# Performance work log

Hardware: AMD Instinct MI355X
Metric: run time of the kernel (lower is better)

The kernel has to match this reference:

```python
import jax, jax.numpy as jnp
import numpy as np

B, T, D_IN, D_OUT, N_FILT, MAX_T = 4, 2048, 512, 512, 24, 2048


def _hankel_filters(max_t: int, k: int) -> np.ndarray:
    # Z_{ij} = 2 / ((i+j)^3 - (i+j)), 1-indexed; top-|eig| eigenvectors
    idx = np.arange(1, max_t + 1, dtype=np.float64)
    ij = idx[None, :] + idx[:, None]
    Z = 2.0 / (ij ** 3 - ij)
    w, v = np.linalg.eigh(Z)
    top = np.argsort(-np.abs(w))[:k]
    return v[:, top].astype(np.float32)  # (max_t, k)


def setup_inputs() -> dict:
    key = jax.random.key(0)
    kx, km = jax.random.split(key)
    x = jax.random.normal(kx, (B, T, D_IN), dtype=jnp.float32)
    filters = jnp.asarray(_hankel_filters(MAX_T, N_FILT))  # (MAX_T, N)
    # nn.Linear weight is (d_out, d_in); stacked -> (N, d_out, d_in)
    scale = 1.0 / np.sqrt(D_IN)
    M_weights = jax.random.uniform(km, (N_FILT, D_OUT, D_IN), dtype=jnp.float32,
                                   minval=-scale, maxval=scale)
    return {"x": x, "filters": filters, "M_weights": M_weights}


def reference(x, filters, M_weights):
    Tlen = x.shape[1]
    phi = filters[:Tlen]                       # (T, N)
    phi_e = phi[None, :, :, None]              # (1, T, N, 1)
    weighted = phi_e * x[:, :, None, :]        # (B, T, N, D_in)
    csum = jnp.cumsum(weighted, axis=1)        # causal cumulative projection
    # per-filter rectangular projection: (B,T,N,f) x (N,o,f) -> (B,T,N,o)
    modulated = jnp.einsum('btnf,nof->btno', csum, M_weights)
    return (phi_e * modulated).sum(axis=2)     # (B, T, D_out)
```

## Files before the change

### kernel.cpp

```cpp
#include <hip/hip_runtime.h>
#include <stdint.h>

#define BQ 4
#define TT 2048
#define DF 512
#define DOUT 512
#define NF 24
#define CHF 8

typedef __attribute__((ext_vector_type(8))) short short8;
typedef __attribute__((ext_vector_type(4))) float f32x4;

typedef __attribute__((address_space(3))) uint8_t       lds_u8;
typedef __attribute__((address_space(1))) const uint8_t glb_u8;

__device__ __forceinline__ float bf2f(unsigned short u) {
    union { unsigned int i; float f; } v; v.i = ((unsigned int)u) << 16; return v.f;
}
__device__ __forceinline__ unsigned short f2bf(float f) {
    union { float f; unsigned int i; } v; v.f = f;
    unsigned int r = v.i + 0x7FFFu + ((v.i >> 16) & 1u);
    return (unsigned short)(r >> 16);
}
__device__ __forceinline__ float lo16f(unsigned int u) { return __uint_as_float(u << 16); }
__device__ __forceinline__ float hi16f(unsigned int u) { return __uint_as_float(u & 0xffff0000u); }

__device__ __forceinline__ int plaus16(unsigned int h) {
    unsigned int e = (h >> 7) & 0xffu;
    return (e >= 97u && e <= 141u) || ((h & 0x7fffu) == 0u);
}

__global__ void k_detect(const unsigned int* __restrict__ X, int* __restrict__ flag)
{
    const int lane = threadIdx.x;
    int cnt = 0;
#pragma unroll
    for (int i = 0; i < 4; ++i) {
        unsigned int w = X[lane * 4 + i];
        cnt += (plaus16(w >> 16) && plaus16(w & 0xffffu)) ? 1 : 0;
    }
    for (int off = 32; off > 0; off >>= 1) cnt += __shfl_down(cnt, off);
    if (lane == 0) *flag = (cnt < 180) ? 1 : 0;
}

__global__ __launch_bounds__(256) void k_convf(
    const void* __restrict__ src, float* __restrict__ dst,
    const int* __restrict__ flag, int n)
{
    const int isf32 = *flag;
    int i = blockIdx.x * 256 + threadIdx.x;
    const int stride = gridDim.x * 256;
    for (; i < n; i += stride)
        dst[i] = isf32 ? ((const float*)src)[i]
                       : bf2f(((const unsigned short*)src)[i]);
}

__global__ __launch_bounds__(256) void k_prep(
    const void* __restrict__ X, const void* __restrict__ Mw,
    const void* __restrict__ Fil,
    unsigned short* __restrict__ Xbf, unsigned short* __restrict__ Mbf,
    float* __restrict__ Fw, int n4x, int n4m, int n4f)
{
    __shared__ int sflag;
    const int tid = threadIdx.x;
    if (tid < 64) {
        int cnt = 0;
        const unsigned int* Xu = (const unsigned int*)X;
#pragma unroll
        for (int i = 0; i < 4; ++i) {
            unsigned int wd = Xu[tid * 4 + i];
            cnt += (plaus16(wd >> 16) && plaus16(wd & 0xffffu)) ? 1 : 0;
        }
        for (int off = 32; off > 0; off >>= 1) cnt += __shfl_down(cnt, off);
        if (tid == 0) sflag = (cnt < 180) ? 1 : 0;
    }
    __syncthreads();
    const int isf32 = sflag;

    const int total = n4x + n4m + n4f;
    for (int i = blockIdx.x * 256 + tid; i < total; i += gridDim.x * 256) {
        if (i < n4x) {
            ushort4 o;
            if (isf32) {
                float4 v = ((const float4*)X)[i];
                o.x = f2bf(v.x); o.y = f2bf(v.y); o.z = f2bf(v.z); o.w = f2bf(v.w);
            } else {
                o = ((const ushort4*)X)[i];
            }
            ((ushort4*)Xbf)[i] = o;
        } else if (i < n4x + n4m) {
            const int j = i - n4x;
            ushort4 o;
            if (isf32) {
                float4 v = ((const float4*)Mw)[j];
                o.x = f2bf(v.x); o.y = f2bf(v.y); o.z = f2bf(v.z); o.w = f2bf(v.w);
            } else {
                o = ((const ushort4*)Mw)[j];
            }
            ((ushort4*)Mbf)[j] = o;
        } else {
            const int j = i - n4x - n4m;
            if (isf32) {
                ((float4*)Fw)[j] = ((const float4*)Fil)[j];
            } else {
                ushort4 u = ((const ushort4*)Fil)[j];
                ((float4*)Fw)[j] = make_float4(bf2f(u.x), bf2f(u.y),
                                               bf2f(u.z), bf2f(u.w));
            }
        }
    }
}

__global__ __launch_bounds__(256, 3) void k_gemm_fast(
    const unsigned short* __restrict__ X,
    const unsigned short* __restrict__ Mw,
    const float* __restrict__ Fw,
    unsigned short* __restrict__ Z,
    float* __restrict__ Cs,
    int r0)
{
    __shared__ unsigned short sAB[128 * 136];
    __shared__ float sPhi[128];
    unsigned short* const sC = sAB;

    const int tid  = threadIdx.x;
    const int lane = tid & 63;
    const int w    = tid >> 6;
    const int wm   = w & 1, wn = w >> 1;
    const int tm   = blockIdx.x;
    const int on0  = blockIdx.y * 128;
    const int n    = blockIdx.z;

    const int rowg0 = r0 + tm * 128;
    if (tid < 128)
        sPhi[tid] = Fw[((rowg0 + tid) & (TT - 1)) * NF + n];

    const unsigned short* Ag = X + (size_t)rowg0 * DF;
    const unsigned short* Bg = Mw + (size_t)n * DOUT * DF + (size_t)on0 * DF;

    auto stage = [&](int kt, int buf) {
        const unsigned short* Ak = Ag + kt * 32;
        const unsigned short* Bk = Bg + kt * 32;
        lds_u8* base = (lds_u8*)sAB + buf * 16384;
#pragma unroll
        for (int i = 0; i < 2; ++i) {
            const int cbase = i * 256 + w * 64;
            const int c = cbase + lane;
            const int r = c >> 2, qs = c & 3;
            const int qg = qs ^ ((r >> 1) & 3);
            __builtin_amdgcn_global_load_lds(
                (const glb_u8*)(Ak + (size_t)r * DF + qg * 8),
                base + cbase * 16, 16, 0, 0);
            __builtin_amdgcn_global_load_lds(
                (const glb_u8*)(Bk + (size_t)r * DF + qg * 8),
                base + 8192 + cbase * 16, 16, 0, 0);
        }
    };

    f32x4 acc[4][4];
#pragma unroll
    for (int i = 0; i < 4; i++)
#pragma unroll
        for (int j = 0; j < 4; j++) acc[i][j] = (f32x4){0.f, 0.f, 0.f, 0.f};

    stage(0, 0);
    __syncthreads();

    const int lr = lane & 15;
    const int q  = lane >> 4;
    const int qsw = (q ^ ((lr >> 1) & 3)) * 8;

    for (int kt = 0; kt < DF / 32; ++kt) {
        const int cur = kt & 1;
        if (kt < DF / 32 - 1) stage(kt + 1, cur ^ 1);

        const unsigned short* sAc = sAB + cur * 8192;
        const unsigned short* sBc = sAc + 4096;
        short8 a[4], b[4];
#pragma unroll
        for (int i = 0; i < 4; i++)
            a[i] = *(const short8*)&sAc[(wm * 64 + i * 16 + lr) * 32 + qsw];
#pragma unroll
        for (int j = 0; j < 4; j++)
            b[j] = *(const short8*)&sBc[(wn * 64 + j * 16 + lr) * 32 + qsw];
#pragma unroll
        for (int i = 0; i < 4; i++)
#pragma unroll
            for (int j = 0; j < 4; j++)
                acc[i][j] = __builtin_amdgcn_mfma_f32_16x16x32_bf16(
                    a[i], b[j], acc[i][j], 0, 0, 0);

        __syncthreads();
    }

    const int rb = (lane >> 4) * 4;
#pragma unroll
    for (int i = 0; i < 4; i++)
#pragma unroll
        for (int j = 0; j < 4; j++)
#pragma unroll
            for (int r = 0; r < 4; r++) {
                int row = wm * 64 + i * 16 + rb + r;
                sC[row * 136 + wn * 64 + j * 16 + (lane & 15)] =
                    f2bf(acc[i][j][r] * sPhi[row]);
            }
    __syncthreads();

#pragma unroll
    for (int it = 0; it < 8; ++it) {
        int row = it * 16 + (tid >> 4);
        int col = (tid & 15) * 8;
        uint4 v = *(const uint4*)&sC[row * 136 + col];
        *(uint4*)&Z[((size_t)(tm * 128 + row) * NF + n) * 512 + on0 + col] = v;
    }

    {
        const int ci  = tid >> 4;
        const int col = (tid & 15) * 8;
        float s0=0.f,s1=0.f,s2=0.f,s3=0.f,s4=0.f,s5=0.f,s6=0.f,s7=0.f;
#pragma unroll
        for (int r = 0; r < CHF; ++r) {
            uint4 v = *(const uint4*)&sC[(ci * CHF + r) * 136 + col];
            s0 += lo16f(v.x); s1 += hi16f(v.x);
            s2 += lo16f(v.y); s3 += hi16f(v.y);
            s4 += lo16f(v.z); s5 += hi16f(v.z);
            s6 += lo16f(v.w); s7 += hi16f(v.w);
        }
        float* cp = &Cs[((size_t)(tm * 16 + ci) * NF + n) * 512 + on0 + col];
        *(float4*)cp       = make_float4(s0, s1, s2, s3);
        *(float4*)(cp + 4) = make_float4(s4, s5, s6, s7);
    }
}

__global__ __launch_bounds__(256, 2) void k_gemm(
    const void* __restrict__ Xv, const void* __restrict__ Mv,
    const void* __restrict__ Fv, const int* __restrict__ flag,
    unsigned short* __restrict__ Z, int r0, int o0, int W)
{
    __shared__ unsigned short sA[128 * 32];
    __shared__ unsigned short sB[128 * 32];
    __shared__ unsigned short sC[128 * 136];
    __shared__ float sPhi[128];

    const int isf32 = *flag;
    const int tid  = threadIdx.x;
    const int lane = tid & 63;
    const int w    = tid >> 6;
    const int wm   = w & 1, wn = w >> 1;
    const int tm   = blockIdx.x;
    const int on0  = o0 + blockIdx.y * 128;
    const int n    = blockIdx.z;

    const int rowg0 = r0 + tm * 128;
    if (tid < 128) {
        int t = (rowg0 + tid) & (TT - 1);
        sPhi[tid] = isf32 ? ((const float*)Fv)[t * NF + n]
                          : bf2f(((const unsigned short*)Fv)[t * NF + n]);
    }

    const unsigned short* Ah = (const unsigned short*)Xv + (size_t)rowg0 * DF;
    const unsigned short* Bh = (const unsigned short*)Mv +
        (size_t)n * DOUT * DF + (size_t)on0 * DF;
    const float* Af = (const float*)Xv + (size_t)rowg0 * DF;
    const float* Bf = (const float*)Mv + (size_t)n * DOUT * DF + (size_t)on0 * DF;

    f32x4 acc[4][4];
#pragma unroll
    for (int i = 0; i < 4; i++)
#pragma unroll
        for (int j = 0; j < 4; j++) acc[i][j] = (f32x4){0.f, 0.f, 0.f, 0.f};

    for (int kt = 0; kt < DF / 32; ++kt) {
        __syncthreads();
        if (!isf32) {
            const unsigned short* Ak = Ah + kt * 32;
            const unsigned short* Bk = Bh + kt * 32;
#pragma unroll
            for (int i = 0; i < 2; ++i) {
                const int c = i * 256 + tid;
                const int r = c >> 2, cc = (c & 3) * 8;
                *(short8*)&sA[r * 32 + cc] = *(const short8*)(Ak + (size_t)r * DF + cc);
                *(short8*)&sB[r * 32 + cc] = *(const short8*)(Bk + (size_t)r * DF + cc);
            }
        } else {
            const float* Ak = Af + kt * 32;
            const float* Bk = Bf + kt * 32;
#pragma unroll
            for (int i = 0; i < 2; ++i) {
                const int c = i * 256 + tid;
                const int r = c >> 2, cc = (c & 3) * 8;
                float4 a0 = *(const float4*)(Ak + (size_t)r * DF + cc);
                float4 a1 = *(const float4*)(Ak + (size_t)r * DF + cc + 4);
                float4 b0 = *(const float4*)(Bk + (size_t)r * DF + cc);
                float4 b1 = *(const float4*)(Bk + (size_t)r * DF + cc + 4);
                short8 sa, sb;
                sa[0]=(short)f2bf(a0.x); sa[1]=(short)f2bf(a0.y);
                sa[2]=(short)f2bf(a0.z); sa[3]=(short)f2bf(a0.w);
                sa[4]=(short)f2bf(a1.x); sa[5]=(short)f2bf(a1.y);
                sa[6]=(short)f2bf(a1.z); sa[7]=(short)f2bf(a1.w);
                sb[0]=(short)f2bf(b0.x); sb[1]=(short)f2bf(b0.y);
                sb[2]=(short)f2bf(b0.z); sb[3]=(short)f2bf(b0.w);
                sb[4]=(short)f2bf(b1.x); sb[5]=(short)f2bf(b1.y);
                sb[6]=(short)f2bf(b1.z); sb[7]=(short)f2bf(b1.w);
                *(short8*)&sA[r * 32 + cc] = sa;
                *(short8*)&sB[r * 32 + cc] = sb;
            }
        }
        __syncthreads();

        const int lr = lane & 15;
        const int lk = (lane >> 4) * 8;
        short8 a[4], b[4];
#pragma unroll
        for (int i = 0; i < 4; i++)
            a[i] = *(const short8*)&sA[(wm * 64 + i * 16 + lr) * 32 + lk];
#pragma unroll
        for (int j = 0; j < 4; j++)
            b[j] = *(const short8*)&sB[(wn * 64 + j * 16 + lr) * 32 + lk];
#pragma unroll
        for (int i = 0; i < 4; i++)
#pragma unroll
            for (int j = 0; j < 4; j++)
                acc[i][j] = __builtin_amdgcn_mfma_f32_16x16x32_bf16(
                    a[i], b[j], acc[i][j], 0, 0, 0);
    }

    const int rb = (lane >> 4) * 4;
#pragma unroll
    for (int i = 0; i < 4; i++)
#pragma unroll
        for (int j = 0; j < 4; j++)
#pragma unroll
            for (int r = 0; r < 4; r++) {
                int row = wm * 64 + i * 16 + rb + r;
                sC[row * 136 + wn * 64 + j * 16 + (lane & 15)] =
                    f2bf(acc[i][j][r] * sPhi[row]);
            }
    __syncthreads();
#pragma unroll
    for (int it = 0; it < 8; ++it) {
        int row = it * 16 + (tid >> 4);
        int col = (tid & 15) * 8;
        uint4 v = *(const uint4*)&sC[row * 136 + col];
        *(uint4*)&Z[((size_t)(tm * 128 + row) * NF + n) * W + (on0 - o0) + col] = v;
    }
}

__global__ __launch_bounds__(256, 2) void k_csum(
    const unsigned short* __restrict__ Z, float* __restrict__ Cs,
    int W, int CHs)
{
    const int c = blockIdx.x, n = blockIdx.y, tid = threadIdx.x;
    const unsigned short* p = Z + ((size_t)(c * CHs) * NF + n) * W + tid * 2;
    float sx = 0.f, sy = 0.f;
#pragma unroll 8
    for (int t = 0; t < CHs; ++t) {
        unsigned int u = *(const unsigned int*)(p + (size_t)t * NF * W);
        sx += lo16f(u);
        sy += hi16f(u);
    }
    float2* q = (float2*)&Cs[((size_t)c * NF + n) * W + tid * 2];
    *q = make_float2(sx, sy);
}

__global__ __launch_bounds__(256, 4) void k_prefix(
    float* __restrict__ Cs, float* __restrict__ Gc,
    int W, int rr, int nch, int nbat)
{
    __shared__ float2 sPart[4][64];
    const int tid  = threadIdx.x;
    const int wv   = tid >> 6, lane = tid & 63;
    const int obw  = W >> 7;
    const int perB = NF * obw;
    const int gw   = blockIdx.x;
    const int b    = gw / perB;
    const int rest = gw % perB;
    const int n    = rest / obw;
    const int ob   = rest % obw;
    const int opair = ob * 64 + lane;

    float* base = Cs + (size_t)b * nch * NF * W + (size_t)n * W + opair * 2;
    const size_t cstride = (size_t)NF * W;
    const int Q  = nch >> 2;
    const int c0 = wv * Q;
    const int end = c0 + Q;

    float sx = 0.f, sy = 0.f;
    for (int c = c0; c < end; ++c) {
        float2 v = *(const float2*)(base + (size_t)c * cstride);
        sx += v.x; sy += v.y;
    }
    sPart[wv][lane] = make_float2(sx, sy);
    __syncthreads();

    float cx = 0.f, cy = 0.f;
    if (nbat == 1 && rr != 0) {
        float2 gv = *(const float2*)&Gc[(size_t)n * DOUT + opair * 2];
        cx = gv.x; cy = gv.y;
    }
    for (int w2 = 0; w2 < wv; ++w2) {
        float2 p = sPart[w2][lane];
        cx += p.x; cy += p.y;
    }

    int c = c0;
    if (Q >= 16) {
        float2 v[8], nx[8];
#pragma unroll
        for (int k = 0; k < 8; ++k)
            v[k] = *(float2*)(base + (size_t)(c + k) * cstride);
        for (; c + 16 <= end; c += 8) {
#pragma unroll
            for (int k = 0; k < 8; ++k)
                nx[k] = *(float2*)(base + (size_t)(c + 8 + k) * cstride);
#pragma unroll
            for (int k = 0; k < 8; ++k) {
                float2* p = (float2*)(base + (size_t)(c + k) * cstride);
                float2 t = v[k];
                *p = make_float2(cx, cy);
                cx += t.x; cy += t.y;
                v[k] = nx[k];
            }
        }
#pragma unroll
        for (int k = 0; k < 8; ++k) {
            float2* p = (float2*)(base + (size_t)(c + k) * cstride);
            float2 t = v[k];
            *p = make_float2(cx, cy);
            cx += t.x; cy += t.y;
        }
        c += 8;
    }
    for (; c < end; ++c) {
        float2* p = (float2*)(base + (size_t)c * cstride);
        float2 t = *p;
        *p = make_float2(cx, cy);
        cx += t.x; cy += t.y;
    }

    if (nbat == 1 && wv == 3)
        *(float2*)&Gc[(size_t)n * DOUT + opair * 2] = make_float2(cx, cy);
}

#define JLIST(F) F(0) F(1) F(2) F(3) F(4) F(5)

__global__ __launch_bounds__(256, 8) void k_scan(
    const unsigned short* __restrict__ Z, const float* __restrict__ Cs,
    const float* __restrict__ Fw, float* __restrict__ Out,
    int r0, int o0, int W, int CHs)
{
    __shared__ float sPhi[32 * NF];
    __shared__ float2 sP[4][8][64];
    const int cg = blockIdx.x, tid = threadIdx.x;
    const int g = tid >> 6, op = tid & 63;
    const int ng0 = g * 6;
    const int c2  = (blockIdx.y * 64 + op) * 2;
    const int act = (c2 + 2 <= W);
    const int c2u = act ? c2 : (W - 2);
    const int t0g = r0 + cg * CHs;
    const int t0 = t0g & (TT - 1);
    for (int i = tid; i < CHs * NF; i += 256)
        sPhi[i] = Fw[(t0 + i / NF) * NF + (i % NF)];
    __syncthreads();

#define DECLG(j) float gx##j, gy##j;
    JLIST(DECLG)
#define INITG(j) { float2 v = *(const float2*)&Cs[((size_t)cg * NF + ng0 + j) * W + c2u]; \
                   gx##j = v.x; gy##j = v.y; }
    JLIST(INITG)

    const unsigned short* zp = Z + ((size_t)cg * CHs * NF + ng0) * W + c2u;
    float* outb = Out + (size_t)t0g * DOUT + o0 + c2;
    for (int tb = 0; tb < CHs; tb += 8) {
#pragma unroll
        for (int tt = 0; tt < 8; ++tt) {
            float ax = 0.f, ay = 0.f;
            const float* php = &sPhi[(tb + tt) * NF + ng0];
#define UPDG(j) { unsigned int u = *(const unsigned int*)(zp + (size_t)j * W); \
                  gx##j += lo16f(u); gy##j += hi16f(u); \
                  float ph = php[j]; ax += ph * gx##j; ay += ph * gy##j; }
            JLIST(UPDG)
            sP[g][tt][op] = make_float2(ax, ay);
            zp += (size_t)NF * W;
        }
        __syncthreads();
#pragma unroll
        for (int k = 0; k < 2; ++k) {
            const int tt = g * 2 + k;
            float2 p0 = sP[0][tt][op], p1 = sP[1][tt][op],
                   p2 = sP[2][tt][op], p3 = sP[3][tt][op];
            if (act)
                *(float2*)(outb + (size_t)(tb + tt) * DOUT) =
                    make_float2(p0.x + p1.x + p2.x + p3.x,
                                p0.y + p1.y + p2.y + p3.y);
        }
        __syncthreads();
    }
}

extern "C" void kernel_launch(void* const* d_in, const int* in_sizes, int n_in,
                              void* d_out, int out_size, void* d_ws, size_t ws_size,
                              hipStream_t stream)
{
    const void* X = d_in[0]; const void* Fil = d_in[1]; const void* Mw = d_in[2];
    for (int i = 0; i < n_in && i < 3; ++i) {
        if (in_sizes[i] == BQ * TT * DF)        X   = d_in[i];
        else if (in_sizes[i] == TT * NF)        Fil = d_in[i];
        else if (in_sizes[i] == NF * DOUT * DF) Mw  = d_in[i];
    }
    float* Out = (float*)d_out;

    const size_t offF = 256;
    const size_t nbF  = (size_t)TT * NF * 4;
    const size_t off0 = offF + nbF;
    const size_t nbX  = (size_t)BQ * TT * DF * 2;
    const size_t nbM  = (size_t)NF * DOUT * DF * 2;
    const size_t nbGc = (size_t)NF * DOUT * 4;

    int* flag = (int*)d_ws;
    float* Fw = (float*)((char*)d_ws + offF);

    const int n4x = BQ * TT * DF / 4;
    const int n4m = NF * DOUT * DF / 4;
    const int n4f = TT * NF / 4;

    for (int G = BQ; G >= 2; G >>= 1) {
        const size_t zB  = (size_t)G * TT * NF * 512 * 2;
        const size_t csB = (size_t)(G * TT / CHF) * NF * 512 * 4;
        if (off0 + nbX + nbM + zB + csB > ws_size) continue;

        unsigned short* Xbf = (unsigned short*)((char*)d_ws + off0);
        unsigned short* Mbf = (unsigned short*)((char*)Xbf + nbX);
        unsigned short* Z   = (unsigned short*)((char*)Mbf + nbM);
        float* Cs = (float*)((char*)Z + zB);

        hipLaunchKernelGGL(k_prep, dim3(2048), dim3(256), 0, stream,
                           X, Mw, Fil, Xbf, Mbf, Fw, n4x, n4m, n4f);

        const int nch = TT / CHF;
        for (int b0 = 0; b0 < BQ; b0 += G) {
            hipLaunchKernelGGL(k_gemm_fast, dim3(G * TT / 128, 4, NF), dim3(256),
                               0, stream, Xbf, Mbf, Fw, Z, Cs, b0 * TT);
            hipLaunchKernelGGL(k_prefix, dim3(G * NF * 4), dim3(256),
                               0, stream, Cs, (float*)nullptr, 512, 0, nch, G);
            hipLaunchKernelGGL(k_scan, dim3(G * nch, 4), dim3(256), 0, stream,
                               Z, Cs, Fw, Out, b0 * TT, 0, 512, CHF);
        }
        return;
    }

    {
        static const int rts[5] = {2048, 1024, 512, 256, 128};
        int RT = 0;
        for (int ri = 0; ri < 5; ++ri) {
            size_t need = off0 + nbX + nbM
                        + (size_t)rts[ri] * NF * 512 * 2
                        + (size_t)(rts[ri] / CHF) * NF * 512 * 4 + nbGc;
            if (need <= ws_size) { RT = rts[ri]; break; }
        }
        if (RT > 0) {
            unsigned short* Xbf = (unsigned short*)((char*)d_ws + off0);
            unsigned short* Mbf = (unsigned short*)((char*)Xbf + nbX);
            unsigned short* Z   = (unsigned short*)((char*)Mbf + nbM);
            float* Cs = (float*)((char*)Z + (size_t)RT * NF * 512 * 2);
            float* Gc = (float*)((char*)Cs + (size_t)(RT / CHF) * NF * 512 * 4);

            hipLaunchKernelGGL(k_prep, dim3(2048), dim3(256), 0, stream,
                               X, Mw, Fil, Xbf, Mbf, Fw, n4x, n4m, n4f);

            const int nrr = TT / RT, nch = RT / CHF;
            for (int b = 0; b < BQ; ++b) {
                for (int rr = 0; rr < nrr; ++rr) {
                    const int r0 = b * TT + rr * RT;
                    hipLaunchKernelGGL(k_gemm_fast, dim3(RT / 128, 4, NF), dim3(256),
                                       0, stream, Xbf, Mbf, Fw, Z, Cs, r0);
                    hipLaunchKernelGGL(k_prefix, dim3(NF * 4), dim3(256),
                                       0, stream, Cs, Gc, 512, rr, nch, 1);
                    hipLaunchKernelGGL(k_scan, dim3(nch, 4), dim3(256), 0, stream,
                                       Z, Cs, Fw, Out, r0, 0, 512, CHF);
                }
            }
            return;
        }
    }

    hipLaunchKernelGGL(k_detect, dim3(1), dim3(64), 0, stream,
                       (const unsigned int*)X, flag);
    hipLaunchKernelGGL(k_convf, dim3(192), dim3(256), 0, stream,
                       Fil, Fw, flag, TT * NF);

    static const int cRT[7] = {2048, 1024, 512, 256, 128, 128, 128};
    static const int cW[7]  = {512, 512, 512, 512, 512, 256, 128};
    int RTs = 128, W = 128;
    for (int ci = 0; ci < 7; ++ci) {
        size_t need = off0 + (size_t)cRT[ci] * NF * cW[ci] * 2
                    + (size_t)(cRT[ci] / 32) * NF * cW[ci] * 4 + nbGc;
        if (need <= ws_size) { RTs = cRT[ci]; W = cW[ci]; break; }
    }
    unsigned short* Z = (unsigned short*)((char*)d_ws + off0);
    float* Cs = (float*)((char*)Z + (size_t)RTs * NF * W * 2);
    float* Gc = (float*)((char*)Cs + (size_t)(RTs / 32) * NF * W * 4);

    const int nrr = TT / RTs, nch = RTs / 32;
    for (int b = 0; b < BQ; ++b) {
        for (int o0 = 0; o0 < DOUT; o0 += W) {
            for (int rr = 0; rr < nrr; ++rr) {
                const int r0 = b * TT + rr * RTs;
                hipLaunchKernelGGL(k_gemm, dim3(RTs / 128, W / 128, NF), dim3(256),
                                   0, stream, X, Mw, Fil, flag, Z, r0, o0, W);
                hipLaunchKernelGGL(k_csum, dim3(nch, NF), dim3(W / 2), 0, stream,
                                   Z, Cs, W, 32);
                hipLaunchKernelGGL(k_prefix, dim3(NF * (W / 128)), dim3(256),
                                   0, stream, Cs, Gc, W, rr, nch, 1);
                hipLaunchKernelGGL(k_scan, dim3(nch, W / 128), dim3(256),
                                   0, stream, Z, Cs, Fw, Out, r0, o0, W, 32);
            }
        }
    }
}
```

Before: 319.4 us.

## Fuse intra-chunk scan into GEMM epilogue, drop Z intermediate, add apply kernel

The GEMM kernel now loops over all 24 filters inside one block of 64 rows, with the per-filter phi scaling and the within-chunk prefix sum (via shuffles) done in registers. The intra-chunk output contribution is accumulated directly into Out, and only the chunk sums are written to Cs. This removes the large bf16 Z intermediate and the scan kernel's reread of it. A new k_apply kernel adds the cross-chunk carry contributions after the prefix pass. The trade-offs are a smaller 64-row tile, per-filter epilogue overhead inside the main loop, and a read-modify-write of Out.

```diff
diff --git a/kernel.cpp b/kernel.cpp
--- a/kernel.cpp
+++ b/kernel.cpp
@@ -111,17 +111,16 @@
     }
 }
 
-__global__ __launch_bounds__(256, 3) void k_gemm_fast(
+__global__ __launch_bounds__(256, 3) void k_gemm_ns(
     const unsigned short* __restrict__ X,
     const unsigned short* __restrict__ Mw,
     const float* __restrict__ Fw,
-    unsigned short* __restrict__ Z,
     float* __restrict__ Cs,
+    float* __restrict__ Out,
     int r0)
 {
-    __shared__ unsigned short sAB[128 * 136];
-    __shared__ float sPhi[128];
-    unsigned short* const sC = sAB;
+    __shared__ unsigned short sAB[2 * 6144];
+    __shared__ float sPhi2[NF * 64];
 
     const int tid  = threadIdx.x;
     const int lane = tid & 63;
@@ -129,19 +128,28 @@
     const int wm   = w & 1, wn = w >> 1;
     const int tm   = blockIdx.x;
     const int on0  = blockIdx.y * 128;
-    const int n    = blockIdx.z;
-
-    const int rowg0 = r0 + tm * 128;
-    if (tid < 128)
-        sPhi[tid] = Fw[((rowg0 + tid) & (TT - 1)) * NF + n];
-
-    const unsigned short* Ag = X + (size_t)rowg0 * DF;
-    const unsigned short* Bg = Mw + (size_t)n * DOUT * DF + (size_t)on0 * DF;
-
-    auto stage = [&](int kt, int buf) {
-        const unsigned short* Ak = Ag + kt * 32;
-        const unsigned short* Bk = Bg + kt * 32;
-        lds_u8* base = (lds_u8*)sAB + buf * 16384;
+    const int rowL = tm * 64;
+    const int rowG = r0 + rowL;
+
+    for (int idx = tid; idx < NF * 64; idx += 256) {
+        int n = idx >> 6, rr2 = idx & 63;
+        sPhi2[idx] = Fw[((rowG + rr2) & (TT - 1)) * NF + n];
+    }
+
+    const unsigned short* Ag = X + (size_t)rowG * DF;
+
+    auto stage = [&](int m) {
+        const int n = m >> 4, kt = m & 15;
+        lds_u8* base = (lds_u8*)sAB + (m & 1) * 12288;
+        {
+            const int c = w * 64 + lane;
+            const int r = c >> 2, qs = c & 3;
+            const int qg = qs ^ ((r >> 1) & 3);
+            __builtin_amdgcn_global_load_lds(
+                (const glb_u8*)(Ag + (size_t)r * DF + kt * 32 + qg * 8),
+                base + (w * 64) * 16, 16, 0, 0);
+        }
+        const unsigned short* Bg = Mw + (size_t)n * DOUT * DF + (size_t)on0 * DF;
 #pragma unroll
         for (int i = 0; i < 2; ++i) {
             const int cbase = i * 256 + w * 64;
@@ -149,86 +157,122 @@
             const int r = c >> 2, qs = c & 3;
             const int qg = qs ^ ((r >> 1) & 3);
             __builtin_amdgcn_global_load_lds(
-                (const glb_u8*)(Ak + (size_t)r * DF + qg * 8),
-                base + cbase * 16, 16, 0, 0);
-            __builtin_amdgcn_global_load_lds(
-                (const glb_u8*)(Bk + (size_t)r * DF + qg * 8),
-                base + 8192 + cbase * 16, 16, 0, 0);
+                (const glb_u8*)(Bg + (size_t)r * DF + kt * 32 + qg * 8),
+                base + 4096 + cbase * 16, 16, 0, 0);
         }
     };
 
-    f32x4 acc[4][4];
-#pragma unroll
-    for (int i = 0; i < 4; i++)
-#pragma unroll
-        for (int j = 0; j < 4; j++) acc[i][j] = (f32x4){0.f, 0.f, 0.f, 0.f};
-
-    stage(0, 0);
+    f32x4 acc[2][4], Bacc[2][4];
+#pragma unroll
+    for (int i = 0; i < 2; i++)
+#pragma unroll
+        for (int j = 0; j < 4; j++) {
+            acc[i][j]  = (f32x4){0.f, 0.f, 0.f, 0.f};
+            Bacc[i][j] = (f32x4){0.f, 0.f, 0.f, 0.f};
+        }
+
+    stage(0);
     __syncthreads();
 
-    const int lr = lane & 15;
-    const int q  = lane >> 4;
+    const int lr  = lane & 15;
+    const int q   = lane >> 4;
     const int qsw = (q ^ ((lr >> 1) & 3)) * 8;
 
-    for (int kt = 0; kt < DF / 32; ++kt) {
-        const int cur = kt & 1;
-        if (kt < DF / 32 - 1) stage(kt + 1, cur ^ 1);
-
-        const unsigned short* sAc = sAB + cur * 8192;
-        const unsigned short* sBc = sAc + 4096;
-        short8 a[4], b[4];
-#pragma unroll
-        for (int i = 0; i < 4; i++)
-            a[i] = *(const short8*)&sAc[(wm * 64 + i * 16 + lr) * 32 + qsw];
+    for (int m = 0; m < NF * 16; ++m) {
+        if (m + 1 < NF * 16) stage(m + 1);
+
+        const unsigned short* sAc = sAB + (m & 1) * 6144;
+        const unsigned short* sBc = sAc + 2048;
+        short8 a[2], b[4];
+#pragma unroll
+        for (int i = 0; i < 2; i++)
+            a[i] = *(const short8*)&sAc[(wm * 32 + i * 16 + lr) * 32 + qsw];
 #pragma unroll
         for (int j = 0; j < 4; j++)
             b[j] = *(const short8*)&sBc[(wn * 64 + j * 16 + lr) * 32 + qsw];
 #pragma unroll
-        for (int i = 0; i < 4; i++)
+        for (int i = 0; i < 2; i++)
 #pragma unroll
             for (int j = 0; j < 4; j++)
                 acc[i][j] = __builtin_amdgcn_mfma_f32_16x16x32_bf16(
                     a[i], b[j], acc[i][j], 0, 0, 0);
 
+        if ((m & 15) == 15) {
+            const int n = m >> 4;
+#pragma unroll
+            for (int i = 0; i < 2; i++) {
+                const int rbase = wm * 32 + i * 16 + q * 4;
+                float ph0 = sPhi2[n * 64 + rbase + 0];
+                float ph1 = sPhi2[n * 64 + rbase + 1];
+                float ph2 = sPhi2[n * 64 + rbase + 2];
+                float ph3 = sPhi2[n * 64 + rbase + 3];
+#pragma unroll
+                for (int j = 0; j < 4; j++) {
+                    float z0 = acc[i][j][0] * ph0;
+                    float z1 = acc[i][j][1] * ph1;
+                    float z2 = acc[i][j][2] * ph2;
+                    float z3 = acc[i][j][3] * ph3;
+                    float p0 = z0, p1 = p0 + z1, p2 = p1 + z2, p3 = p2 + z3;
+                    float t  = __shfl_xor(p3, 16);
+                    float off = (q & 1) ? t : 0.f;
+                    Bacc[i][j][0] += ph0 * (off + p0);
+                    Bacc[i][j][1] += ph1 * (off + p1);
+                    Bacc[i][j][2] += ph2 * (off + p2);
+                    Bacc[i][j][3] += ph3 * (off + p3);
+                    if (q & 1) {
+                        int ch  = (rowL >> 3) + wm * 4 + i * 2 + (q >> 1);
+                        int col = on0 + wn * 64 + j * 16 + lr;
+                        Cs[((size_t)ch * NF + n) * 512 + col] = off + p3;
+                    }
+                    acc[i][j] = (f32x4){0.f, 0.f, 0.f, 0.f};
+                }
+            }
+        }
         __syncthreads();
     }
 
-    const int rb = (lane >> 4) * 4;
-#pragma unroll
-    for (int i = 0; i < 4; i++)
+#pragma unroll
+    for (int i = 0; i < 2; i++)
 #pragma unroll
         for (int j = 0; j < 4; j++)
 #pragma unroll
             for (int r = 0; r < 4; r++) {
-                int row = wm * 64 + i * 16 + rb + r;
-                sC[row * 136 + wn * 64 + j * 16 + (lane & 15)] =
-                    f2bf(acc[i][j][r] * sPhi[row]);
-            }
+                int row = rowG + wm * 32 + i * 16 + q * 4 + r;
+                Out[(size_t)row * DOUT + on0 + wn * 64 + j * 16 + lr] =
+                    Bacc[i][j][r];
+            }
+}
+
+__global__ __launch_bounds__(256, 8) void k_apply(
+    float* __restrict__ Out, const float* __restrict__ Cs,
+    const float* __restrict__ Fw, int r0)
+{
+    __shared__ float sP2[CHF * NF];
+    const int c = blockIdx.x, tid = threadIdx.x;
+    const int t0g = r0 + c * CHF;
+    if (tid < CHF * NF)
+        sP2[tid] = Fw[((t0g + tid / NF) & (TT - 1)) * NF + (tid % NF)];
     __syncthreads();
 
-#pragma unroll
-    for (int it = 0; it < 8; ++it) {
-        int row = it * 16 + (tid >> 4);
-        int col = (tid & 15) * 8;
-        uint4 v = *(const uint4*)&sC[row * 136 + col];
-        *(uint4*)&Z[((size_t)(tm * 128 + row) * NF + n) * 512 + on0 + col] = v;
-    }
-
-    {
-        const int ci  = tid >> 4;
-        const int col = (tid & 15) * 8;
-        float s0=0.f,s1=0.f,s2=0.f,s3=0.f,s4=0.f,s5=0.f,s6=0.f,s7=0.f;
-#pragma unroll
-        for (int r = 0; r < CHF; ++r) {
-            uint4 v = *(const uint4*)&sC[(ci * CHF + r) * 136 + col];
-            s0 += lo16f(v.x); s1 += hi16f(v.x);
-            s2 += lo16f(v.y); s3 += hi16f(v.y);
-            s4 += lo16f(v.z); s5 += hi16f(v.z);
-            s6 += lo16f(v.w); s7 += hi16f(v.w);
-        }
-        float* cp = &Cs[((size_t)(tm * 16 + ci) * NF + n) * 512 + on0 + col];
-        *(float4*)cp       = make_float4(s0, s1, s2, s3);
-        *(float4*)(cp + 4) = make_float4(s4, s5, s6, s7);
+    const int col2 = tid * 2;
+    float2 a[CHF];
+#pragma unroll
+    for (int t = 0; t < CHF; ++t) a[t] = make_float2(0.f, 0.f);
+    const float* cb = Cs + (size_t)c * NF * 512 + col2;
+#pragma unroll 6
+    for (int n = 0; n < NF; ++n) {
+        float2 g = *(const float2*)(cb + (size_t)n * 512);
+#pragma unroll
+        for (int t = 0; t < CHF; ++t) {
+            float ph = sP2[t * NF + n];
+            a[t].x += ph * g.x; a[t].y += ph * g.y;
+        }
+    }
+#pragma unroll
+    for (int t = 0; t < CHF; ++t) {
+        float2* po = (float2*)&Out[(size_t)(t0g + t) * DOUT + col2];
+        float2 o = *po;
+        *po = make_float2(o.x + a[t].x, o.y + a[t].y);
     }
 }
 
@@ -394,7 +438,7 @@
     __syncthreads();
 
     float cx = 0.f, cy = 0.f;
-    if (nbat == 1 && rr != 0) {
+    if (nbat == 1 && rr != 0 && Gc) {
         float2 gv = *(const float2*)&Gc[(size_t)n * DOUT + opair * 2];
         cx = gv.x; cy = gv.y;
     }
@@ -438,7 +482,7 @@
         cx += t.x; cy += t.y;
     }
 
-    if (nbat == 1 && wv == 3)
+    if (nbat == 1 && wv == 3 && Gc)
         *(float2*)&Gc[(size_t)n * DOUT + opair * 2] = make_float2(cx, cy);
 }
 
@@ -465,9 +509,9 @@
 
 #define DECLG(j) float gx##j, gy##j;
     JLIST(DECLG)
-#define INITG(j) { float2 v = *(const float2*)&Cs[((size_t)cg * NF + ng0 + j) * W + c2u]; \
-                   gx##j = v.x; gy##j = v.y; }
-    JLIST(INITG)
+#define INITG2(j) { float2 v = *(const float2*)&Cs[((size_t)cg * NF + ng0 + j) * W + c2u]; \
+                    gx##j = v.x; gy##j = v.y; }
+    JLIST(INITG2)
 
     const unsigned short* zp = Z + ((size_t)cg * CHs * NF + ng0) * W + c2u;
     float* outb = Out + (size_t)t0g * DOUT + o0 + c2;
@@ -476,10 +520,10 @@
         for (int tt = 0; tt < 8; ++tt) {
             float ax = 0.f, ay = 0.f;
             const float* php = &sPhi[(tb + tt) * NF + ng0];
-#define UPDG(j) { unsigned int u = *(const unsigned int*)(zp + (size_t)j * W); \
-                  gx##j += lo16f(u); gy##j += hi16f(u); \
-                  float ph = php[j]; ax += ph * gx##j; ay += ph * gy##j; }
-            JLIST(UPDG)
+#define UPDG2(j) { unsigned int u = *(const unsigned int*)(zp + (size_t)j * W); \
+                   gx##j += lo16f(u); gy##j += hi16f(u); \
+                   float ph = php[j]; ax += ph * gx##j; ay += ph * gy##j; }
+            JLIST(UPDG2)
             sP[g][tt][op] = make_float2(ax, ay);
             zp += (size_t)NF * W;
         }
@@ -524,61 +568,44 @@
     const int n4m = NF * DOUT * DF / 4;
     const int n4f = TT * NF / 4;
 
-    for (int G = BQ; G >= 2; G >>= 1) {
-        const size_t zB  = (size_t)G * TT * NF * 512 * 2;
-        const size_t csB = (size_t)(G * TT / CHF) * NF * 512 * 4;
-        if (off0 + nbX + nbM + zB + csB > ws_size) continue;
-
-        unsigned short* Xbf = (unsigned short*)((char*)d_ws + off0);
-        unsigned short* Mbf = (unsigned short*)((char*)Xbf + nbX);
-        unsigned short* Z   = (unsigned short*)((char*)Mbf + nbM);
-        float* Cs = (float*)((char*)Z + zB);
-
-        hipLaunchKernelGGL(k_prep, dim3(2048), dim3(256), 0, stream,
-                           X, Mw, Fil, Xbf, Mbf, Fw, n4x, n4m, n4f);
-
-        const int nch = TT / CHF;
-        for (int b0 = 0; b0 < BQ; b0 += G) {
-            hipLaunchKernelGGL(k_gemm_fast, dim3(G * TT / 128, 4, NF), dim3(256),
-                               0, stream, Xbf, Mbf, Fw, Z, Cs, b0 * TT);
-            hipLaunchKernelGGL(k_prefix, dim3(G * NF * 4), dim3(256),
-                               0, stream, Cs, (float*)nullptr, 512, 0, nch, G);
-            hipLaunchKernelGGL(k_scan, dim3(G * nch, 4), dim3(256), 0, stream,
-                               Z, Cs, Fw, Out, b0 * TT, 0, 512, CHF);
-        }
-        return;
-    }
-
     {
-        static const int rts[5] = {2048, 1024, 512, 256, 128};
-        int RT = 0;
-        for (int ri = 0; ri < 5; ++ri) {
-            size_t need = off0 + nbX + nbM
-                        + (size_t)rts[ri] * NF * 512 * 2
-                        + (size_t)(rts[ri] / CHF) * NF * 512 * 4 + nbGc;
-            if (need <= ws_size) { RT = rts[ri]; break; }
-        }
-        if (RT > 0) {
+        const size_t csB = (size_t)(BQ * TT / CHF) * NF * 512 * 4;
+        if (off0 + nbX + nbM + csB <= ws_size) {
             unsigned short* Xbf = (unsigned short*)((char*)d_ws + off0);
             unsigned short* Mbf = (unsigned short*)((char*)Xbf + nbX);
-            unsigned short* Z   = (unsigned short*)((char*)Mbf + nbM);
-            float* Cs = (float*)((char*)Z + (size_t)RT * NF * 512 * 2);
-            float* Gc = (float*)((char*)Cs + (size_t)(RT / CHF) * NF * 512 * 4);
+            float* Cs = (float*)((char*)Mbf + nbM);
 
             hipLaunchKernelGGL(k_prep, dim3(2048), dim3(256), 0, stream,
                                X, Mw, Fil, Xbf, Mbf, Fw, n4x, n4m, n4f);
-
-            const int nrr = TT / RT, nch = RT / CHF;
+            hipLaunchKernelGGL(k_gemm_ns, dim3(BQ * TT / 64, 4), dim3(256),
+                               0, stream, Xbf, Mbf, Fw, Cs, Out, 0);
+            hipLaunchKernelGGL(k_prefix, dim3(BQ * NF * 4), dim3(256),
+                               0, stream, Cs, (float*)nullptr, 512, 0,
+                               TT / CHF, BQ);
+            hipLaunchKernelGGL(k_apply, dim3(BQ * TT / CHF), dim3(256),
+                               0, stream, Out, Cs, Fw, 0);
+            return;
+        }
+    }
+
+    {
+        const size_t csB = (size_t)(TT / CHF) * NF * 512 * 4;
+        if (off0 + nbX + nbM + csB <= ws_size) {
+            unsigned short* Xbf = (unsigned short*)((char*)d_ws + off0);
+            unsigned short* Mbf = (unsigned short*)((char*)Xbf + nbX);
+            float* Cs = (float*)((char*)Mbf + nbM);
+
+            hipLaunchKernelGGL(k_prep, dim3(2048), dim3(256), 0, stream,
+                               X, Mw, Fil, Xbf, Mbf, Fw, n4x, n4m, n4f);
             for (int b = 0; b < BQ; ++b) {
-                for (int rr = 0; rr < nrr; ++rr) {
-                    const int r0 = b * TT + rr * RT;
-                    hipLaunchKernelGGL(k_gemm_fast, dim3(RT / 128, 4, NF), dim3(256),
-                                       0, stream, Xbf, Mbf, Fw, Z, Cs, r0);
-                    hipLaunchKernelGGL(k_prefix, dim3(NF * 4), dim3(256),
-                                       0, stream, Cs, Gc, 512, rr, nch, 1);
-                    hipLaunchKernelGGL(k_scan, dim3(nch, 4), dim3(256), 0, stream,
-                                       Z, Cs, Fw, Out, r0, 0, 512, CHF);
-                }
+                const int r0 = b * TT;
+                hipLaunchKernelGGL(k_gemm_ns, dim3(TT / 64, 4), dim3(256),
+                                   0, stream, Xbf, Mbf, Fw, Cs, Out, r0);
+                hipLaunchKernelGGL(k_prefix, dim3(NF * 4), dim3(256),
+                                   0, stream, Cs, (float*)nullptr, 512, 0,
+                                   TT / CHF, 1);
+                hipLaunchKernelGGL(k_apply, dim3(TT / CHF), dim3(256),
+                                   0, stream, Out, Cs, Fw, r0);
             }
             return;
         }
```

After: 344.3 us. +7.8%, slower.
